# Performance work log

Measured on AMD Instinct MI355X. Metric: run time of the kernel, lower is better.

Reference implementation:

```python
import jax, jax.numpy as jnp
import numpy as np

B, L, H, K = 16, 2048, 1024, 4  # batch, seq, hidden, heads
NEG = -1e9  # stand-in for -inf in masked softmax (grad-safe, prob ~0)

def setup_inputs() -> dict:
    key = jax.random.key(0)
    ks = jax.random.split(key, 6)
    s = 0.02
    hidden = jax.random.normal(ks[0], (B, L, H), dtype=jnp.float32)
    masks = jax.random.randint(ks[1], (B, L), 0, 2).astype(jnp.bool_)
    Wp = jax.random.normal(ks[2], (H, H * K), dtype=jnp.float32) * s
    W1 = jax.random.normal(ks[3], (K, H, H // 2), dtype=jnp.float32) * s
    b1 = jax.random.normal(ks[4], (K, H // 2), dtype=jnp.float32) * s
    W2 = jax.random.normal(ks[5], (K, H // 2), dtype=jnp.float32) * s
    return {"hidden": hidden, "masks": masks, "Wp": Wp, "W1": W1, "b1": b1, "W2": W2}

def reference(hidden, masks, Wp, W1, b1, W2):
    b, l, h = hidden.shape
    k = W1.shape[0]
    # projection (no bias), split into heads: [b,l,k,h]
    proj = (hidden @ Wp).reshape(b, l, k, h)
    # per-head tanh MLP score: Linear(h, h//2)+bias -> tanh -> Linear(h//2, 1)
    a1 = jnp.tanh(jnp.einsum('blkh,khd->blkd', proj, W1) + b1)  # [b,l,k,h//2]
    logits = jnp.einsum('blkd,kd->kbl', a1, W2)                 # [k,b,l]
    # masked softmax over sequence dim
    logits = jnp.where(masks[None, :, :], NEG, logits)
    attn = jax.nn.softmax(logits, axis=-1)                      # [k,b,l]
    return attn
```

## Files before the change

kernel.cpp:

```cpp
#include <hip/hip_runtime.h>
#include <hip/hip_bf16.h>
#include <cstdint>
#include <cstddef>

#define HD   1024
#define NK   4
#define DD   512
#define LSEQ 2048
#define NB   16
#define MTOT (NB*LSEQ)
#define NF2  (NK*DD)

typedef __attribute__((ext_vector_type(4))) float f32x4;
typedef __attribute__((ext_vector_type(8))) short bf16x8;

#define GLOAD16(gp, lp) __builtin_amdgcn_global_load_lds( \
    (const __attribute__((address_space(1))) void*)(gp),  \
    (__attribute__((address_space(3))) void*)(lp), 16, 0, 0)

static __device__ __forceinline__ ushort f2bf(float f) {
  union { float f; unsigned u; } x; x.f = f;
  unsigned r = x.u + 0x7FFFu + ((x.u >> 16) & 1u);
  return (ushort)(r >> 16);
}

static __device__ __forceinline__ float fast_tanh(float x) {
  x = fminf(fmaxf(x, -15.f), 15.f);
  float t = __expf(2.0f * x);
  return (t - 1.0f) / (t + 1.0f);
}

__global__ void detect_mask_kernel(const unsigned char* __restrict__ m, int nbytes,
                                   int* __restrict__ flag) {
  int found = 0;
  for (int i = blockIdx.x * blockDim.x + threadIdx.x; i < nbytes;
       i += gridDim.x * blockDim.x)
    if ((i & 3) && m[i]) found = 1;
  if (__any(found) && (threadIdx.x & 63) == 0) atomicOr(flag, 1);
}

__global__ void cvt_f32_bf16_kernel(const float* __restrict__ src,
                                    ushort* __restrict__ dst, long n) {
  long stride = (long)gridDim.x * blockDim.x * 4;
  for (long i = ((long)blockIdx.x * blockDim.x + threadIdx.x) * 4; i < n; i += stride) {
    f32x4 v = *(const f32x4*)(src + i);
    ushort4 o; o.x = f2bf(v.x); o.y = f2bf(v.y); o.z = f2bf(v.z); o.w = f2bf(v.w);
    *(ushort4*)(dst + i) = o;
  }
}

__global__ void cvt_wp_heads_kernel(const float* __restrict__ Wp,
                                    ushort* __restrict__ WpH) {
  long i4 = ((long)blockIdx.x * blockDim.x + threadIdx.x) * 4;
  int h = (int)(i4 >> 20);
  int c = (int)((i4 >> 10) & 1023);
  int j = (int)(i4 & 1023);
  f32x4 v = *(const f32x4*)(Wp + (long)c * (NK * HD) + h * HD + j);
  ushort4 o; o.x = f2bf(v.x); o.y = f2bf(v.y); o.z = f2bf(v.z); o.w = f2bf(v.w);
  *(ushort4*)(WpH + i4) = o;
}

__global__ void transpose_cvt_kernel(const float* __restrict__ src,
                                     ushort* __restrict__ dst,
                                     int R, int C, long sBatch, long dBatch) {
  __shared__ float tile[32][33];
  const float* s = src + blockIdx.z * sBatch;
  ushort* d = dst + blockIdx.z * dBatch;
  int c0 = blockIdx.x * 32, r0 = blockIdx.y * 32;
  int tx = threadIdx.x, ty = threadIdx.y;
  #pragma unroll
  for (int i = 0; i < 32; i += 8)
    tile[ty + i][tx] = s[(long)(r0 + ty + i) * C + (c0 + tx)];
  __syncthreads();
  #pragma unroll
  for (int i = 0; i < 32; i += 8)
    d[(long)(c0 + ty + i) * R + (r0 + tx)] = f2bf(tile[tx][ty + i]);
}

template<int MODE>
__global__ __launch_bounds__(256, 2)
void gemm128_kernel(const ushort* __restrict__ A, int lda, long aZs,
                    const ushort* __restrict__ Bt, int ldb, long bZs, int Kdim,
                    ushort* __restrict__ Cout, int ldc, long cZs,
                    const float* __restrict__ b1, const float* __restrict__ W2,
                    float* __restrict__ partialOut, int m0glob) {
  __shared__ __align__(16) char lds[16384];

  const int tid = threadIdx.x;
  const int wave = tid >> 6, lane = tid & 63;
  const int z = blockIdx.z;

  const int bid = blockIdx.x + gridDim.x * blockIdx.y;
  const int nMB = gridDim.x, nNB = gridDim.y;
  int m0, n0;
  if ((nMB & 7) == 0) {
    const int x = bid & 7, j = bid >> 3;
    m0 = (x * (nMB >> 3) + j / nNB) * 128;
    n0 = (j % nNB) * 128;
  } else {
    m0 = (bid % nMB) * 128; n0 = (bid / nMB) * 128;
  }

  const ushort* Ag = A + z * aZs + (long)m0 * lda;
  const ushort* Bg = Bt + z * bZs + (long)n0 * ldb;

  const int wr = wave >> 1, wc = wave & 1;
  const int rsel = lane & 15, ch = lane >> 4;
  const int chunkC = (ch ^ ((rsel >> 1) & 3)) << 4;
  const int laneA = wr * 4096 + rsel * 64 + chunkC;
  const int laneB = 8192 + wc * 4096 + rsel * 64 + chunkC;

  const int stRow = wave * 16 + (lane >> 2);
  const int stCg = ((lane & 3) ^ ((lane >> 3) & 3)) * 8;
  const int ldsOff = wave * 1024;

  f32x4 acc[4][4] = {};

  const int ksteps = Kdim >> 5;
  for (int kt = 0; kt < ksteps; ++kt) {
    const int kk = (kt << 5) + stCg;
    GLOAD16(Ag + (long)(m0 ? 0 : 0, stRow) * lda + kk,        (char*)lds + ldsOff);
    GLOAD16(Ag + (long)(64 + stRow) * lda + kk,               (char*)lds + 4096 + ldsOff);
    GLOAD16(Bg + (long)(stRow) * ldb + kk,                    (char*)lds + 8192 + ldsOff);
    GLOAD16(Bg + (long)(64 + stRow) * ldb + kk,               (char*)lds + 12288 + ldsOff);
    __syncthreads();

    bf16x8 aF[4], bF[4];
    #pragma unroll
    for (int mf = 0; mf < 4; ++mf)
      aF[mf] = *(const bf16x8*)(lds + laneA + mf * 1024);
    #pragma unroll
    for (int nf = 0; nf < 4; ++nf)
      bF[nf] = *(const bf16x8*)(lds + laneB + nf * 1024);
    #pragma unroll
    for (int mf = 0; mf < 4; ++mf)
      #pragma unroll
      for (int nf = 0; nf < 4; ++nf)
        acc[mf][nf] = __builtin_amdgcn_mfma_f32_16x16x32_bf16(
            aF[mf], bF[nf], acc[mf][nf], 0, 0, 0);
    __syncthreads();
  }

  if constexpr (MODE == 0) {
    #pragma unroll
    for (int mf = 0; mf < 4; ++mf)
      #pragma unroll
      for (int nf = 0; nf < 4; ++nf) {
        const int col = n0 + wc * 64 + nf * 16 + (lane & 15);
        #pragma unroll
        for (int r = 0; r < 4; ++r) {
          const int row = m0 + wr * 64 + mf * 16 + ((lane >> 4) << 2) + r;
          Cout[z * cZs + (long)row * ldc + col] = f2bf(acc[mf][nf][r]);
        }
      }
  } else {
    float b1v[4], w2v[4];
    #pragma unroll
    for (int nf = 0; nf < 4; ++nf) {
      const int col = n0 + wc * 64 + nf * 16 + (lane & 15);
      b1v[nf] = b1[col];
      w2v[nf] = W2[col];
    }
    const int wslice = (n0 + wc * 64) >> 6;
    float* pb = partialOut + (long)wslice * MTOT + m0glob + m0 + wr * 64;
    #pragma unroll
    for (int mf = 0; mf < 4; ++mf)
      #pragma unroll
      for (int r = 0; r < 4; ++r) {
        float s = 0.f;
        #pragma unroll
        for (int nf = 0; nf < 4; ++nf)
          s += fast_tanh(acc[mf][nf][r] + b1v[nf]) * w2v[nf];
        s += __shfl_xor(s, 1, 64);
        s += __shfl_xor(s, 2, 64);
        s += __shfl_xor(s, 4, 64);
        s += __shfl_xor(s, 8, 64);
        if ((lane & 15) == 0)
          pb[mf * 16 + ((lane >> 4) << 2) + r] = s;
      }
  }
}

__global__ __launch_bounds__(256)
void masked_softmax_kernel(const float* __restrict__ partial,
                           const unsigned char* __restrict__ maskB,
                           const int* __restrict__ maskI,
                           const int* __restrict__ flag,
                           float* __restrict__ out) {
  const int kb = blockIdx.x;
  const int k = kb >> 4, b = kb & (NB - 1);
  const long base = (long)kb * LSEQ;
  const bool isByte = (*flag != 0);
  const int tid = threadIdx.x;
  const float* pk = partial + (long)(k * 8) * MTOT + (long)b * LSEQ;

  float x[8];
  float mx = -3.0e38f;
  #pragma unroll
  for (int j = 0; j < 8; ++j) {
    int l = tid + j * 256;
    float v = 0.f;
    #pragma unroll
    for (int ws = 0; ws < 8; ++ws) v += pk[(long)ws * MTOT + l];
    bool msk = isByte ? (maskB[b * LSEQ + l] != 0) : (maskI[b * LSEQ + l] != 0);
    v = msk ? -1e9f : v;
    x[j] = v; mx = fmaxf(mx, v);
  }
  __shared__ float redm[4], reds[4];
  #pragma unroll
  for (int off = 32; off >= 1; off >>= 1) mx = fmaxf(mx, __shfl_xor(mx, off, 64));
  if ((tid & 63) == 0) redm[tid >> 6] = mx;
  __syncthreads();
  mx = fmaxf(fmaxf(redm[0], redm[1]), fmaxf(redm[2], redm[3]));

  float sum = 0.f;
  #pragma unroll
  for (int j = 0; j < 8; ++j) { x[j] = __expf(x[j] - mx); sum += x[j]; }
  #pragma unroll
  for (int off = 32; off >= 1; off >>= 1) sum += __shfl_xor(sum, off, 64);
  if ((tid & 63) == 0) reds[tid >> 6] = sum;
  __syncthreads();
  sum = reds[0] + reds[1] + reds[2] + reds[3];

  float inv = 1.0f / sum;
  #pragma unroll
  for (int j = 0; j < 8; ++j) out[base + tid + j * 256] = x[j] * inv;
}

extern "C" void kernel_launch(void* const* d_in, const int* in_sizes, int n_in,
                              void* d_out, int out_size, void* d_ws, size_t ws_size,
                              hipStream_t stream) {
  const float* hidden = (const float*)d_in[0];
  const void*  masks  = d_in[1];
  const float* Wp     = (const float*)d_in[2];
  const float* W1     = (const float*)d_in[3];
  const float* b1     = (const float*)d_in[4];
  const float* W2     = (const float*)d_in[5];
  float* out = (float*)d_out;

  char* ws = (char*)d_ws;
  ushort* W1T      = (ushort*)(ws + 0);
  ushort* WpH      = (ushort*)(ws + 4194304);
  ushort* WfT      = (ushort*)(ws + 12582912);
  float*  partial  = (float*) (ws + 16777216);
  int*    flag     = (int*)   (ws + 20971520);
  ushort* hiddenBf = (ushort*)(ws + 20971776);

  const size_t fixedBytes = 20971776;
  size_t avail = (ws_size > fixedBytes) ? (ws_size - fixedBytes) : 0;
  long chunkM = (long)(avail / ((long)HD * 2)) & ~127L;
  if (chunkM > MTOT) chunkM = MTOT;
  if (chunkM < 128) chunkM = 128;

  hipMemsetAsync(flag, 0, 256, stream);

  detect_mask_kernel<<<8, 256, 0, stream>>>((const unsigned char*)masks, NB * LSEQ, flag);

  dim3 tb(32, 8);
  transpose_cvt_kernel<<<dim3(DD / 32, HD / 32, NK), tb, 0, stream>>>(
      W1, W1T, HD, DD, (long)HD * DD, (long)DD * HD);
  cvt_wp_heads_kernel<<<4096, 256, 0, stream>>>(Wp, WpH);

  gemm128_kernel<0><<<dim3(DD / 128, HD / 128, NK), 256, 0, stream>>>(
      W1T, HD, (long)DD * HD,
      WpH, HD, (long)HD * HD, HD,
      WfT, HD, (long)DD * HD,
      nullptr, nullptr, nullptr, 0);

  for (long m0 = 0; m0 < MTOT; m0 += chunkM) {
    long cm = chunkM; if (m0 + cm > MTOT) cm = MTOT - m0;
    cvt_f32_bf16_kernel<<<2048, 256, 0, stream>>>(
        hidden + m0 * HD, hiddenBf, cm * HD);
    gemm128_kernel<1><<<dim3(cm / 128, NF2 / 128, 1), 256, 0, stream>>>(
        hiddenBf, HD, 0,
        WfT, HD, 0, HD,
        nullptr, 0, 0,
        b1, W2, partial, (int)m0);
  }

  masked_softmax_kernel<<<NK * NB, 256, 0, stream>>>(
      partial, (const unsigned char*)masks, (const int*)masks, flag, out);
}
```

Before: 255.6 us.

## Fuse fp32-to-bf16 conversion of hidden into the main GEMM A-tile load

The main GEMM now loads fp32 hidden rows directly into LDS with a swizzled layout and converts them to packed bf16 when building MFMA fragments. This removes the separate conversion kernel, the bf16 staging buffer in workspace, and the chunked launch loop. The trade-off is doubled A-tile bytes per k-step, a larger LDS allocation, and extra conversion ALU work inside the inner loop.

Result: slower. 277.4 us (+8.6%).

```diff
diff --git a/kernel.cpp b/kernel.cpp
--- a/kernel.cpp
+++ b/kernel.cpp
@@ -24,6 +24,12 @@
   return (ushort)(r >> 16);
 }
 
+static __device__ __forceinline__ unsigned pkbf(float a, float b) {
+  float2 t; t.x = a; t.y = b;
+  __hip_bfloat162 h = __float22bfloat162_rn(t);
+  return *reinterpret_cast<unsigned*>(&h);
+}
+
 static __device__ __forceinline__ float fast_tanh(float x) {
   x = fminf(fmaxf(x, -15.f), 15.f);
   float t = __expf(2.0f * x);
@@ -37,16 +43,6 @@
        i += gridDim.x * blockDim.x)
     if ((i & 3) && m[i]) found = 1;
   if (__any(found) && (threadIdx.x & 63) == 0) atomicOr(flag, 1);
-}
-
-__global__ void cvt_f32_bf16_kernel(const float* __restrict__ src,
-                                    ushort* __restrict__ dst, long n) {
-  long stride = (long)gridDim.x * blockDim.x * 4;
-  for (long i = ((long)blockIdx.x * blockDim.x + threadIdx.x) * 4; i < n; i += stride) {
-    f32x4 v = *(const f32x4*)(src + i);
-    ushort4 o; o.x = f2bf(v.x); o.y = f2bf(v.y); o.z = f2bf(v.z); o.w = f2bf(v.w);
-    *(ushort4*)(dst + i) = o;
-  }
 }
 
 __global__ void cvt_wp_heads_kernel(const float* __restrict__ Wp,
@@ -77,14 +73,15 @@
     d[(long)(c0 + ty + i) * R + (r0 + tx)] = f2bf(tile[tx][ty + i]);
 }
 
-template<int MODE>
+template<int MODE, int AF32>
 __global__ __launch_bounds__(256, 2)
-void gemm128_kernel(const ushort* __restrict__ A, int lda, long aZs,
+void gemm128_kernel(const void* __restrict__ A, int lda, long aZs,
                     const ushort* __restrict__ Bt, int ldb, long bZs, int Kdim,
                     ushort* __restrict__ Cout, int ldc, long cZs,
                     const float* __restrict__ b1, const float* __restrict__ W2,
                     float* __restrict__ partialOut, int m0glob) {
-  __shared__ __align__(16) char lds[16384];
+  __shared__ __align__(16) char lds[AF32 ? 24576 : 16384];
+  constexpr int AB = AF32 ? 16384 : 8192;
 
   const int tid = threadIdx.x;
   const int wave = tid >> 6, lane = tid & 63;
@@ -101,34 +98,62 @@
     m0 = (bid % nMB) * 128; n0 = (bid / nMB) * 128;
   }
 
-  const ushort* Ag = A + z * aZs + (long)m0 * lda;
-  const ushort* Bg = Bt + z * bZs + (long)n0 * ldb;
+  const float*  Agf = (const float*)A  + z * aZs + (long)m0 * lda;
+  const ushort* Agb = (const ushort*)A + z * aZs + (long)m0 * lda;
+  const ushort* Bg  = Bt + z * bZs + (long)n0 * ldb;
 
   const int wr = wave >> 1, wc = wave & 1;
   const int rsel = lane & 15, ch = lane >> 4;
+
   const int chunkC = (ch ^ ((rsel >> 1) & 3)) << 4;
-  const int laneA = wr * 4096 + rsel * 64 + chunkC;
-  const int laneB = 8192 + wc * 4096 + rsel * 64 + chunkC;
-
-  const int stRow = wave * 16 + (lane >> 2);
+  const int laneB = AB + wc * 4096 + rsel * 64 + chunkC;
+  const int sA = rsel & 7;
+  const int laneA0 = (wr * 64 + rsel) * 128 + (((ch * 2)     ^ sA) << 4);
+  const int laneA1 = (wr * 64 + rsel) * 128 + (((ch * 2 + 1) ^ sA) << 4);
+  const int laneAb = wr * 4096 + rsel * 64 + chunkC;
+
+  const int stRowA = wave * 8 + (lane >> 3);
+  const int cSrcA = (((lane & 7) ^ ((lane >> 3) & 7))) * 4;
+  const int stRowB = wave * 16 + (lane >> 2);
   const int stCg = ((lane & 3) ^ ((lane >> 3) & 3)) * 8;
-  const int ldsOff = wave * 1024;
 
   f32x4 acc[4][4] = {};
 
   const int ksteps = Kdim >> 5;
   for (int kt = 0; kt < ksteps; ++kt) {
-    const int kk = (kt << 5) + stCg;
-    GLOAD16(Ag + (long)(m0 ? 0 : 0, stRow) * lda + kk,        (char*)lds + ldsOff);
-    GLOAD16(Ag + (long)(64 + stRow) * lda + kk,               (char*)lds + 4096 + ldsOff);
-    GLOAD16(Bg + (long)(stRow) * ldb + kk,                    (char*)lds + 8192 + ldsOff);
-    GLOAD16(Bg + (long)(64 + stRow) * ldb + kk,               (char*)lds + 12288 + ldsOff);
+    if constexpr (AF32) {
+      const int kk32 = (kt << 5) + cSrcA;
+      #pragma unroll
+      for (int i = 0; i < 4; ++i)
+        GLOAD16(Agf + (long)(i * 32 + stRowA) * lda + kk32,
+                (char*)lds + i * 4096 + wave * 1024);
+      const int kkb = (kt << 5) + stCg;
+      GLOAD16(Bg + (long)stRowB * ldb + kkb,        (char*)lds + AB + wave * 1024);
+      GLOAD16(Bg + (long)(64 + stRowB) * ldb + kkb, (char*)lds + AB + 4096 + wave * 1024);
+    } else {
+      const int kk = (kt << 5) + stCg;
+      GLOAD16(Agb + (long)stRowB * lda + kk,        (char*)lds + wave * 1024);
+      GLOAD16(Agb + (long)(64 + stRowB) * lda + kk, (char*)lds + 4096 + wave * 1024);
+      GLOAD16(Bg + (long)stRowB * ldb + kk,         (char*)lds + AB + wave * 1024);
+      GLOAD16(Bg + (long)(64 + stRowB) * ldb + kk,  (char*)lds + AB + 4096 + wave * 1024);
+    }
     __syncthreads();
 
     bf16x8 aF[4], bF[4];
-    #pragma unroll
-    for (int mf = 0; mf < 4; ++mf)
-      aF[mf] = *(const bf16x8*)(lds + laneA + mf * 1024);
+    if constexpr (AF32) {
+      #pragma unroll
+      for (int mf = 0; mf < 4; ++mf) {
+        f32x4 va = *(const f32x4*)(lds + laneA0 + mf * 2048);
+        f32x4 vb = *(const f32x4*)(lds + laneA1 + mf * 2048);
+        unsigned* ap = (unsigned*)&aF[mf];
+        ap[0] = pkbf(va[0], va[1]); ap[1] = pkbf(va[2], va[3]);
+        ap[2] = pkbf(vb[0], vb[1]); ap[3] = pkbf(vb[2], vb[3]);
+      }
+    } else {
+      #pragma unroll
+      for (int mf = 0; mf < 4; ++mf)
+        aF[mf] = *(const bf16x8*)(lds + laneAb + mf * 1024);
+    }
     #pragma unroll
     for (int nf = 0; nf < 4; ++nf)
       bF[nf] = *(const bf16x8*)(lds + laneB + nf * 1024);
@@ -244,13 +269,6 @@
   ushort* WfT      = (ushort*)(ws + 12582912);
   float*  partial  = (float*) (ws + 16777216);
   int*    flag     = (int*)   (ws + 20971520);
-  ushort* hiddenBf = (ushort*)(ws + 20971776);
-
-  const size_t fixedBytes = 20971776;
-  size_t avail = (ws_size > fixedBytes) ? (ws_size - fixedBytes) : 0;
-  long chunkM = (long)(avail / ((long)HD * 2)) & ~127L;
-  if (chunkM > MTOT) chunkM = MTOT;
-  if (chunkM < 128) chunkM = 128;
 
   hipMemsetAsync(flag, 0, 256, stream);
 
@@ -261,22 +279,17 @@
       W1, W1T, HD, DD, (long)HD * DD, (long)DD * HD);
   cvt_wp_heads_kernel<<<4096, 256, 0, stream>>>(Wp, WpH);
 
-  gemm128_kernel<0><<<dim3(DD / 128, HD / 128, NK), 256, 0, stream>>>(
+  gemm128_kernel<0, 0><<<dim3(DD / 128, HD / 128, NK), 256, 0, stream>>>(
       W1T, HD, (long)DD * HD,
       WpH, HD, (long)HD * HD, HD,
       WfT, HD, (long)DD * HD,
       nullptr, nullptr, nullptr, 0);
 
-  for (long m0 = 0; m0 < MTOT; m0 += chunkM) {
-    long cm = chunkM; if (m0 + cm > MTOT) cm = MTOT - m0;
-    cvt_f32_bf16_kernel<<<2048, 256, 0, stream>>>(
-        hidden + m0 * HD, hiddenBf, cm * HD);
-    gemm128_kernel<1><<<dim3(cm / 128, NF2 / 128, 1), 256, 0, stream>>>(
-        hiddenBf, HD, 0,
-        WfT, HD, 0, HD,
-        nullptr, 0, 0,
-        b1, W2, partial, (int)m0);
-  }
+  gemm128_kernel<1, 1><<<dim3(MTOT / 128, NF2 / 128, 1), 256, 0, stream>>>(
+      hidden, HD, 0,
+      WfT, HD, 0, HD,
+      nullptr, 0, 0,
+      b1, W2, partial, 0);
 
   masked_softmax_kernel<<<NK * NB, 256, 0, stream>>>(
       partial, (const unsigned char*)masks, (const int*)masks, flag, out);
```
